# Kernel tuning notes

Measured on AMD Instinct MI355X. Metric: run time of the kernel, lower is better.

## Reference

```python
import jax, jax.numpy as jnp
import numpy as np

D_K = 1024
HEADS = 16
HK = 64
HV = 64


def setup_inputs() -> dict:
    key = jax.random.key(0)
    ks = jax.random.split(key, 12)
    B, S = 4, 2048
    sc_in = 1.0 / np.sqrt(D_K)
    sc_u = 1.0 / np.sqrt(HV * HEADS)
    return {
        "q": jax.random.normal(ks[0], (B, S, D_K), jnp.float32),
        "k": jax.random.normal(ks[1], (B, S, D_K), jnp.float32),
        "v": jax.random.normal(ks[2], (B, S, D_K), jnp.float32),
        "Wq": jax.random.normal(ks[3], (D_K, HK * HEADS), jnp.float32) * sc_in,
        "bq": jax.random.normal(ks[4], (HK * HEADS,), jnp.float32) * sc_in,
        "Wk": jax.random.normal(ks[5], (D_K, HK * HEADS), jnp.float32) * sc_in,
        "bk": jax.random.normal(ks[6], (HK * HEADS,), jnp.float32) * sc_in,
        "Wv": jax.random.normal(ks[7], (D_K, HV * HEADS), jnp.float32) * sc_in,
        "bv": jax.random.normal(ks[8], (HV * HEADS,), jnp.float32) * sc_in,
        "Wu": jax.random.normal(ks[9], (HV * HEADS, D_K), jnp.float32) * sc_u,
        "bu": jax.random.normal(ks[10], (D_K,), jnp.float32) * sc_u,
    }


def reference(q, k, v, Wq, bq, Wk, bk, Wv, bv, Wu, bu):
    B, S, _ = q.shape
    # QKV projections, split heads: (B, S, H, dh) -> (B, H, S, dh)
    qh = (q @ Wq + bq).reshape(B, S, HEADS, HK).transpose(0, 2, 1, 3)
    kh = (k @ Wk + bk).reshape(B, S, HEADS, HK).transpose(0, 2, 1, 3)
    vh = (v @ Wv + bv).reshape(B, S, HEADS, HV).transpose(0, 2, 1, 3)
    # Naive attention: scores scaled by sqrt(head_size) as in Sdpa
    scores = jnp.einsum("bhqd,bhkd->bhqk", qh, kh) / jnp.sqrt(
        jnp.asarray(HK, qh.dtype)
    )
    attn = jax.nn.softmax(scores, axis=-1)
    out = jnp.einsum("bhqk,bhkd->bhqd", attn, vh)  # (B, H, S, HV)
    # Merge heads: (B, S, H*HV), then output projection
    merged = out.transpose(0, 2, 1, 3).reshape(B, S, HEADS * HV)
    return merged @ Wu + bu
```

## Files before the change

kernel.cpp:

```cpp
#include <hip/hip_runtime.h>

typedef __bf16 bf16;
typedef __bf16 bf16x8 __attribute__((ext_vector_type(8)));
typedef __bf16 bf16x4 __attribute__((ext_vector_type(4)));
typedef float  f32x4  __attribute__((ext_vector_type(4)));

#define GLD_LDS16(gp, lp) __builtin_amdgcn_global_load_lds( \
    (const __attribute__((address_space(1))) unsigned int*)(const void*)(gp), \
    (__attribute__((address_space(3))) unsigned int*)(void*)(lp), 16, 0, 0)

constexpr int BB = 4, SSEQ = 2048, DK = 1024, NH = 16, DH = 64;
constexpr int M = BB * SSEQ;

constexpr size_t SZ_X = (size_t)M * DK * 2;
constexpr size_t SZ_W = (size_t)DK * DK * 2;
constexpr size_t OFF_QBF = 0;
constexpr size_t OFF_KBF = OFF_QBF + SZ_X;
constexpr size_t OFF_VBF = OFF_KBF + SZ_X;
constexpr size_t OFF_WQT = OFF_VBF + SZ_X;
constexpr size_t OFF_WKT = OFF_WQT + SZ_W;
constexpr size_t OFF_WVT = OFF_WKT + SZ_W;
constexpr size_t OFF_WUT = OFF_WVT + SZ_W;
constexpr size_t OFF_QH  = OFF_WUT + SZ_W;
constexpr size_t OFF_KH  = OFF_QH + SZ_X;
constexpr size_t OFF_VTH = OFF_KH + SZ_X;
constexpr size_t OFF_MRG = OFF_VTH + SZ_X;

__global__ void cvt_x(const float* __restrict__ q, const float* __restrict__ k,
                      const float* __restrict__ v,
                      bf16* __restrict__ qb, bf16* __restrict__ kb, bf16* __restrict__ vb) {
    const float* s = (blockIdx.z == 0) ? q : (blockIdx.z == 1) ? k : v;
    bf16*        d = (blockIdx.z == 0) ? qb : (blockIdx.z == 1) ? kb : vb;
    size_t i = (size_t)blockIdx.x * blockDim.x + threadIdx.x;
    float4 val = ((const float4*)s)[i];
    bf16x4 o = { (bf16)val.x, (bf16)val.y, (bf16)val.z, (bf16)val.w };
    ((bf16x4*)d)[i] = o;
}

__global__ void cvt_wT(const float* __restrict__ wq, const float* __restrict__ wk,
                       const float* __restrict__ wv, const float* __restrict__ wu,
                       bf16* __restrict__ wqt, bf16* __restrict__ wkt,
                       bf16* __restrict__ wvt, bf16* __restrict__ wut) {
    const float* w = (blockIdx.z == 0) ? wq : (blockIdx.z == 1) ? wk
                   : (blockIdx.z == 2) ? wv : wu;
    bf16* o        = (blockIdx.z == 0) ? wqt : (blockIdx.z == 1) ? wkt
                   : (blockIdx.z == 2) ? wvt : wut;
    __shared__ float t[64][65];
    int tx = threadIdx.x & 63, ty = threadIdx.x >> 6;
    int bx = blockIdx.x * 64, by = blockIdx.y * 64;
#pragma unroll
    for (int r = 0; r < 16; r++) {
        int row = ty * 16 + r;
        t[row][tx] = w[(size_t)(by + row) * DK + bx + tx];
    }
    __syncthreads();
#pragma unroll
    for (int r = 0; r < 16; r++) {
        int row2 = ty * 16 + r;
        o[(size_t)(bx + row2) * DK + by + tx] = (bf16)t[tx][row2];
    }
}

struct GArg {
    const bf16* A; const bf16* BT; const float* bias; void* out; int mode; float oscale;
};

__global__ __launch_bounds__(256, 2) void gemm_bt(GArg g0, GArg g1, GArg g2) {
    GArg g;
    if (blockIdx.z == 0) g = g0; else if (blockIdx.z == 1) g = g1; else g = g2;
    __shared__ __attribute__((aligned(16))) bf16 As[128 * 32];
    __shared__ __attribute__((aligned(16))) bf16 Bs[128 * 32];
    const int tid = threadIdx.x;
    const int lane = tid & 63, wv = tid >> 6;
    const int wm = (wv & 1) * 64, wn = (wv >> 1) * 64;
    const int cl = lane & 15, qd = lane >> 4;
    const int rowbase = blockIdx.y * 128, colbase = blockIdx.x * 128;

    f32x4 acc[4][4];
#pragma unroll
    for (int i = 0; i < 4; i++)
#pragma unroll
        for (int j = 0; j < 4; j++) acc[i][j] = f32x4{0.f, 0.f, 0.f, 0.f};

    const bool swapped = (g.mode == 1);
    for (int k0 = 0; k0 < DK; k0 += 32) {
        __syncthreads();
#pragma unroll
        for (int c = 0; c < 2; c++) {
            int f = (c * 256 + tid) * 8;
            int row = f >> 5, col = f & 31;
            GLD_LDS16(g.A + (size_t)(rowbase + row) * DK + k0 + col, &As[f]);
        }
#pragma unroll
        for (int c = 0; c < 2; c++) {
            int f = (c * 256 + tid) * 8;
            int row = f >> 5, col = f & 31;
            GLD_LDS16(g.BT + (size_t)(colbase + row) * DK + k0 + col, &Bs[f]);
        }
        __syncthreads();
        bf16x8 af[4], bfr[4];
#pragma unroll
        for (int i = 0; i < 4; i++)
            af[i] = *(const bf16x8*)&As[(wm + i * 16 + cl) * 32 + qd * 8];
#pragma unroll
        for (int j = 0; j < 4; j++)
            bfr[j] = *(const bf16x8*)&Bs[(wn + j * 16 + cl) * 32 + qd * 8];
        if (swapped) {
#pragma unroll
            for (int i = 0; i < 4; i++)
#pragma unroll
                for (int j = 0; j < 4; j++)
                    acc[i][j] = __builtin_amdgcn_mfma_f32_16x16x32_bf16(bfr[j], af[i], acc[i][j], 0, 0, 0);
        } else {
#pragma unroll
            for (int i = 0; i < 4; i++)
#pragma unroll
                for (int j = 0; j < 4; j++)
                    acc[i][j] = __builtin_amdgcn_mfma_f32_16x16x32_bf16(af[i], bfr[j], acc[i][j], 0, 0, 0);
        }
    }

    if (g.mode == 2) {
        float* out = (float*)g.out;
#pragma unroll
        for (int i = 0; i < 4; i++)
#pragma unroll
            for (int j = 0; j < 4; j++)
#pragma unroll
                for (int r = 0; r < 4; r++) {
                    int row = rowbase + wm + i * 16 + qd * 4 + r;
                    int col = colbase + wn + j * 16 + cl;
                    out[(size_t)row * DK + col] = (acc[i][j][r] + g.bias[col]) * g.oscale;
                }
    } else if (g.mode == 0) {
        bf16* out = (bf16*)g.out;
#pragma unroll
        for (int i = 0; i < 4; i++)
#pragma unroll
            for (int j = 0; j < 4; j++)
#pragma unroll
                for (int r = 0; r < 4; r++) {
                    int row = rowbase + wm + i * 16 + qd * 4 + r;
                    int col = colbase + wn + j * 16 + cl;
                    float v = (acc[i][j][r] + g.bias[col]) * g.oscale;
                    out[(size_t)row * DK + col] = (bf16)v;
                }
    } else {
        bf16* out = (bf16*)g.out;
#pragma unroll
        for (int i = 0; i < 4; i++)
#pragma unroll
            for (int j = 0; j < 4; j++)
#pragma unroll
                for (int r = 0; r < 4; r++) {
                    int colg = colbase + wn + j * 16 + qd * 4 + r;
                    int rowg = rowbase + wm + i * 16 + cl;
                    int b_ = rowg >> 11, s_ = rowg & 2047;
                    float v = (acc[i][j][r] + g.bias[colg]) * g.oscale;
                    out[((size_t)(b_ * NH + (colg >> 6)) * DH + (colg & 63)) * SSEQ + s_] = (bf16)v;
                }
    }
}

__global__ __launch_bounds__(256, 4) void attn(const bf16* __restrict__ Qh,
                                               const bf16* __restrict__ Kh,
                                               const bf16* __restrict__ VTh,
                                               bf16* __restrict__ mrg) {
    __shared__ __attribute__((aligned(16))) bf16 Ks[2][64 * 64];
    __shared__ __attribute__((aligned(16))) bf16 VTs[2][64 * 64];
    const int tid = threadIdx.x;
    const int lane = tid & 63, w = tid >> 6;
    const int cl = lane & 15, qd = lane >> 4;
    const int F = blockIdx.x;
    const int xcd = F & 7, slot = F >> 3;
    const int bh = xcd * 8 + (slot & 7);
    const int qt = slot >> 3;
    const int b_ = bh >> 4, h_ = bh & 15;
    const int qbase = qt * 128;
    const bf16* Qb = Qh + ((size_t)b_ * SSEQ) * DK + h_ * DH;
    const bf16* Kb = Kh + ((size_t)b_ * SSEQ) * DK + h_ * DH;
    const bf16* Vb = VTh + (size_t)bh * DH * SSEQ;

    bf16x8 qf[2][2];
#pragma unroll
    for (int mi = 0; mi < 2; mi++) {
        int q = qbase + w * 32 + mi * 16 + cl;
        qf[mi][0] = *(const bf16x8*)&Qb[(size_t)q * DK + qd * 8];
        qf[mi][1] = *(const bf16x8*)&Qb[(size_t)q * DK + 32 + qd * 8];
    }
    f32x4 O[2][4];
#pragma unroll
    for (int mi = 0; mi < 2; mi++)
#pragma unroll
        for (int jv = 0; jv < 4; jv++) O[mi][jv] = f32x4{0.f, 0.f, 0.f, 0.f};
    float ps[2] = {0.f, 0.f};

    auto stage = [&](int kt, int buf) {
#pragma unroll
        for (int c = 0; c < 2; c++) {
            int L = c * 256 + tid;
            int row = L >> 3, lc = (L & 7) ^ (row & 7);
            int prow = ((row >> 5) << 5) | (((row >> 2) & 3) << 3)
                     | (((row >> 4) & 1) << 2) | (row & 3);
            GLD_LDS16(Kb + (size_t)(kt * 64 + prow) * DK + lc * 8, &Ks[buf][L * 8]);
        }
#pragma unroll
        for (int c = 0; c < 2; c++) {
            int L = c * 256 + tid;
            int row = L >> 3, lc = (L & 7) ^ (row & 7);
            GLD_LDS16(Vb + (size_t)row * SSEQ + kt * 64 + lc * 8, &VTs[buf][L * 8]);
        }
    };
    stage(0, 0);

    for (int kt = 0; kt < 32; kt++) {
        const int buf = kt & 1;
        __syncthreads();
        if (kt + 1 < 32) stage(kt + 1, buf ^ 1);

        bf16x8 pf8[2][2];
#pragma unroll
        for (int jt = 0; jt < 4; jt++) {
            bf16x8 kf0 = *(const bf16x8*)&Ks[buf][(jt * 16 + cl) * 64 + ((qd ^ (cl & 7)) * 8)];
            bf16x8 kf1 = *(const bf16x8*)&Ks[buf][(jt * 16 + cl) * 64 + (((4 + qd) ^ (cl & 7)) * 8)];
#pragma unroll
            for (int mi = 0; mi < 2; mi++) {
                f32x4 S = __builtin_amdgcn_mfma_f32_16x16x32_bf16(kf0, qf[mi][0],
                                                                  f32x4{0.f, 0.f, 0.f, 0.f}, 0, 0, 0);
                S = __builtin_amdgcn_mfma_f32_16x16x32_bf16(kf1, qf[mi][1], S, 0, 0, 0);
                float s = 0.f;
#pragma unroll
                for (int r = 0; r < 4; r++) {
                    float p = __builtin_amdgcn_exp2f(S[r]);
                    s += p;
                    pf8[mi][jt >> 1][(jt & 1) * 4 + r] = (bf16)p;
                }
                ps[mi] += s;
            }
        }

#pragma unroll
        for (int g = 0; g < 2; g++) {
#pragma unroll
            for (int jv = 0; jv < 4; jv++) {
                bf16x8 vf = *(const bf16x8*)&VTs[buf][(jv * 16 + cl) * 64 +
                                (((g * 4 + qd) ^ (cl & 7)) * 8)];
#pragma unroll
                for (int mi = 0; mi < 2; mi++)
                    O[mi][jv] = __builtin_amdgcn_mfma_f32_16x16x32_bf16(vf, pf8[mi][g], O[mi][jv], 0, 0, 0);
            }
        }
    }

#pragma unroll
    for (int mi = 0; mi < 2; mi++) {
        float t = ps[mi];
        t += __shfl_xor(t, 16);
        t += __shfl_xor(t, 32);
        float inv = 1.0f / t;
        int q = qbase + w * 32 + mi * 16 + cl;
        size_t ro = ((size_t)(b_ * SSEQ + q)) * DK + h_ * DH;
#pragma unroll
        for (int jv = 0; jv < 4; jv++) {
            bf16x4 o4;
#pragma unroll
            for (int r = 0; r < 4; r++) o4[r] = (bf16)(O[mi][jv][r] * inv);
            *(bf16x4*)&mrg[ro + jv * 16 + qd * 4] = o4;
        }
    }
}

extern "C" void kernel_launch(void* const* d_in, const int* in_sizes, int n_in,
                              void* d_out, int out_size, void* d_ws, size_t ws_size,
                              hipStream_t stream) {
    const float* q  = (const float*)d_in[0];
    const float* k  = (const float*)d_in[1];
    const float* v  = (const float*)d_in[2];
    const float* Wq = (const float*)d_in[3];
    const float* bq = (const float*)d_in[4];
    const float* Wk = (const float*)d_in[5];
    const float* bk = (const float*)d_in[6];
    const float* Wv = (const float*)d_in[7];
    const float* bv = (const float*)d_in[8];
    const float* Wu = (const float*)d_in[9];
    const float* bu = (const float*)d_in[10];
    char* ws = (char*)d_ws;
    bf16* qbf = (bf16*)(ws + OFF_QBF);
    bf16* kbf = (bf16*)(ws + OFF_KBF);
    bf16* vbf = (bf16*)(ws + OFF_VBF);
    bf16* wqt = (bf16*)(ws + OFF_WQT);
    bf16* wkt = (bf16*)(ws + OFF_WKT);
    bf16* wvt = (bf16*)(ws + OFF_WVT);
    bf16* wut = (bf16*)(ws + OFF_WUT);
    bf16* qh  = (bf16*)(ws + OFF_QH);
    bf16* kh  = (bf16*)(ws + OFF_KH);
    bf16* vth = (bf16*)(ws + OFF_VTH);
    bf16* mrg = (bf16*)(ws + OFF_MRG);

    cvt_x<<<dim3(8192, 1, 3), 256, 0, stream>>>(q, k, v, qbf, kbf, vbf);
    cvt_wT<<<dim3(16, 16, 4), 256, 0, stream>>>(Wq, Wk, Wv, Wu, wqt, wkt, wvt, wut);

    GArg gq{qbf, wqt, bq, (void*)qh, 0, 0.18033688011112043f};
    GArg gk{kbf, wkt, bk, (void*)kh, 0, 1.0f};
    GArg gv{vbf, wvt, bv, (void*)vth, 1, 1.0f};
    gemm_bt<<<dim3(8, 64, 3), 256, 0, stream>>>(gq, gk, gv);

    attn<<<dim3(1024), 256, 0, stream>>>(qh, kh, vth, mrg);

    GArg go{mrg, wut, bu, d_out, 2, 1.0f};
    gemm_bt<<<dim3(8, 64, 1), 256, 0, stream>>>(go, go, go);
}
```

Measured before the change: 344.1 us.

## Double-buffer GEMM with 128x256 tiles, XOR-swizzled LDS and grouped block order

The bf16 GEMM now uses 512-thread blocks computing 128x256 tiles with a 64-wide k step. A two-stage LDS double buffer is driven by explicit vmcnt waits and barriers, so the next tile's global loads overlap the MFMA work. LDS rows are XOR-swizzled to avoid bank conflicts, and a 1D grid with grouped row mapping is meant to improve L2 reuse. The cost is more LDS per block (96KB), which limits occupancy, plus hand-placed waitcnt logic that depends on exact instruction counts.

```diff
diff --git a/kernel.cpp b/kernel.cpp
--- a/kernel.cpp
+++ b/kernel.cpp
@@ -65,16 +65,19 @@
     const bf16* A; const bf16* BT; const float* bias; void* out; int mode; float oscale;
 };
 
-__global__ __launch_bounds__(256, 2) void gemm_bt(GArg g0, GArg g1, GArg g2) {
+__global__ __launch_bounds__(512, 2) void gemm_bt(GArg g0, GArg g1, GArg g2) {
     GArg g;
     if (blockIdx.z == 0) g = g0; else if (blockIdx.z == 1) g = g1; else g = g2;
-    __shared__ __attribute__((aligned(16))) bf16 As[128 * 32];
-    __shared__ __attribute__((aligned(16))) bf16 Bs[128 * 32];
+    __shared__ __attribute__((aligned(16))) bf16 As[2][128 * 64];
+    __shared__ __attribute__((aligned(16))) bf16 Bs[2][256 * 64];
     const int tid = threadIdx.x;
     const int lane = tid & 63, wv = tid >> 6;
-    const int wm = (wv & 1) * 64, wn = (wv >> 1) * 64;
+    const int wm = (wv >> 2) * 64;
+    const int wn = (wv & 3) * 64;
     const int cl = lane & 15, qd = lane >> 4;
-    const int rowbase = blockIdx.y * 128, colbase = blockIdx.x * 128;
+    const int x = (int)blockIdx.x;
+    const int rowbase = ((x & 7) * 8 + ((x >> 3) & 7)) * 128;
+    const int colbase = (x >> 6) * 256;
 
     f32x4 acc[4][4];
 #pragma unroll
@@ -83,42 +86,82 @@
         for (int j = 0; j < 4; j++) acc[i][j] = f32x4{0.f, 0.f, 0.f, 0.f};
 
     const bool swapped = (g.mode == 1);
-    for (int k0 = 0; k0 < DK; k0 += 32) {
-        __syncthreads();
+
+    auto stage = [&](int t, int buf) {
 #pragma unroll
         for (int c = 0; c < 2; c++) {
-            int f = (c * 256 + tid) * 8;
-            int row = f >> 5, col = f & 31;
-            GLD_LDS16(g.A + (size_t)(rowbase + row) * DK + k0 + col, &As[f]);
-        }
-#pragma unroll
-        for (int c = 0; c < 2; c++) {
-            int f = (c * 256 + tid) * 8;
-            int row = f >> 5, col = f & 31;
-            GLD_LDS16(g.BT + (size_t)(colbase + row) * DK + k0 + col, &Bs[f]);
-        }
-        __syncthreads();
-        bf16x8 af[4], bfr[4];
-#pragma unroll
-        for (int i = 0; i < 4; i++)
-            af[i] = *(const bf16x8*)&As[(wm + i * 16 + cl) * 32 + qd * 8];
+            int L = c * 512 + tid;
+            int row = L >> 3, s16 = L & 7;
+            int sc = s16 ^ (row & 7);
+            GLD_LDS16(g.A + (size_t)(rowbase + row) * DK + t * 64 + sc * 8, &As[buf][L * 8]);
+        }
+#pragma unroll
+        for (int c = 0; c < 4; c++) {
+            int L = c * 512 + tid;
+            int row = L >> 3, s16 = L & 7;
+            int sc = s16 ^ (row & 7);
+            GLD_LDS16(g.BT + (size_t)(colbase + row) * DK + t * 64 + sc * 8, &Bs[buf][L * 8]);
+        }
+    };
+
+    stage(0, 0);
+    stage(1, 1);
+
+    auto ktile = [&](int t, int cur, bool doStage, bool last) __attribute__((always_inline)) {
+        if (last) asm volatile("s_waitcnt vmcnt(0)" ::: "memory");
+        else      asm volatile("s_waitcnt vmcnt(6)" ::: "memory");
+        asm volatile("s_barrier" ::: "memory");
+        bf16x8 a0[4], b0[4], a1[4], b1[4];
+#pragma unroll
+        for (int i = 0; i < 4; i++)
+            a0[i] = *(const bf16x8*)&As[cur][(wm + i * 16 + cl) * 64 + ((qd ^ (cl & 7)) * 8)];
 #pragma unroll
         for (int j = 0; j < 4; j++)
-            bfr[j] = *(const bf16x8*)&Bs[(wn + j * 16 + cl) * 32 + qd * 8];
+            b0[j] = *(const bf16x8*)&Bs[cur][(wn + j * 16 + cl) * 64 + ((qd ^ (cl & 7)) * 8)];
+#pragma unroll
+        for (int i = 0; i < 4; i++)
+            a1[i] = *(const bf16x8*)&As[cur][(wm + i * 16 + cl) * 64 + (((4 + qd) ^ (cl & 7)) * 8)];
+#pragma unroll
+        for (int j = 0; j < 4; j++)
+            b1[j] = *(const bf16x8*)&Bs[cur][(wn + j * 16 + cl) * 64 + (((4 + qd) ^ (cl & 7)) * 8)];
+        __builtin_amdgcn_s_setprio(1);
         if (swapped) {
 #pragma unroll
             for (int i = 0; i < 4; i++)
 #pragma unroll
                 for (int j = 0; j < 4; j++)
-                    acc[i][j] = __builtin_amdgcn_mfma_f32_16x16x32_bf16(bfr[j], af[i], acc[i][j], 0, 0, 0);
+                    acc[i][j] = __builtin_amdgcn_mfma_f32_16x16x32_bf16(b0[j], a0[i], acc[i][j], 0, 0, 0);
         } else {
 #pragma unroll
             for (int i = 0; i < 4; i++)
 #pragma unroll
                 for (int j = 0; j < 4; j++)
-                    acc[i][j] = __builtin_amdgcn_mfma_f32_16x16x32_bf16(af[i], bfr[j], acc[i][j], 0, 0, 0);
-        }
-    }
+                    acc[i][j] = __builtin_amdgcn_mfma_f32_16x16x32_bf16(a0[i], b0[j], acc[i][j], 0, 0, 0);
+        }
+        __builtin_amdgcn_s_setprio(0);
+        asm volatile("s_waitcnt lgkmcnt(0)" ::: "memory");
+        asm volatile("s_barrier" ::: "memory");
+        if (doStage) stage(t + 2, cur);
+        __builtin_amdgcn_s_setprio(1);
+        if (swapped) {
+#pragma unroll
+            for (int i = 0; i < 4; i++)
+#pragma unroll
+                for (int j = 0; j < 4; j++)
+                    acc[i][j] = __builtin_amdgcn_mfma_f32_16x16x32_bf16(b1[j], a1[i], acc[i][j], 0, 0, 0);
+        } else {
+#pragma unroll
+            for (int i = 0; i < 4; i++)
+#pragma unroll
+                for (int j = 0; j < 4; j++)
+                    acc[i][j] = __builtin_amdgcn_mfma_f32_16x16x32_bf16(a1[i], b1[j], acc[i][j], 0, 0, 0);
+        }
+        __builtin_amdgcn_s_setprio(0);
+    };
+
+    for (int t = 0; t < 14; ++t) ktile(t, t & 1, true, false);
+    ktile(14, 0, false, false);
+    ktile(15, 1, false, true);
 
     if (g.mode == 2) {
         float* out = (float*)g.out;
@@ -303,10 +346,10 @@
     GArg gq{qbf, wqt, bq, (void*)qh, 0, 0.18033688011112043f};
     GArg gk{kbf, wkt, bk, (void*)kh, 0, 1.0f};
     GArg gv{vbf, wvt, bv, (void*)vth, 1, 1.0f};
-    gemm_bt<<<dim3(8, 64, 3), 256, 0, stream>>>(gq, gk, gv);
+    gemm_bt<<<dim3(256, 1, 3), 512, 0, stream>>>(gq, gk, gv);
 
     attn<<<dim3(1024), 256, 0, stream>>>(qh, kh, vth, mrg);
 
     GArg go{mrg, wut, bu, d_out, 2, 1.0f};
-    gemm_bt<<<dim3(8, 64, 1), 256, 0, stream>>>(go, go, go);
-}
+    gemm_bt<<<dim3(256, 1, 1), 512, 0, stream>>>(go, go, go);
+}
```

Result: faster. 323.7 us (-5.9%).
